# Kernel optimization log

Hardware: AMD Instinct MI355X
Metric: run time of the kernel (lower is better)

The kernel has to match this reference:

```python
import jax, jax.numpy as jnp
import numpy as np
import math

C = 1.0
IN_FEATURES = 512
SCALE = 1.0 / math.sqrt(IN_FEATURES)  # 1/sqrt(input_size) * lr_mul, lr_mul=1
LR_MUL = 1.0
GAIN = math.sqrt(2.0)
EPS = 1e-5       # clamp epsilon used by hyptorch-style pmath
PROJ_EPS = 1e-3  # boundary epsilon for project()


def _norm(x):
    return jnp.linalg.norm(x, axis=-1, keepdims=True)


def _artanh(x):
    return jnp.arctanh(jnp.clip(x, -1.0 + EPS, 1.0 - EPS))


def _project(x, c):
    sqrt_c = c ** 0.5
    norm = jnp.maximum(_norm(x), EPS)
    maxnorm = (1.0 - PROJ_EPS) / sqrt_c
    return jnp.where(norm > maxnorm, x / norm * maxnorm, x)


def _expmap0(u, c):
    sqrt_c = c ** 0.5
    u_norm = jnp.maximum(_norm(u), EPS)
    return jnp.tanh(sqrt_c * u_norm) * u / (sqrt_c * u_norm)


def _mobius_add(x, y, c):
    x2 = jnp.sum(x * x, axis=-1, keepdims=True)
    y2 = jnp.sum(y * y, axis=-1, keepdims=True)
    xy = jnp.sum(x * y, axis=-1, keepdims=True)
    num = (1.0 + 2.0 * c * xy + c * y2) * x + (1.0 - c * x2) * y
    denom = 1.0 + 2.0 * c * xy + c * c * x2 * y2
    return num / (denom + EPS)


def _mobius_matvec(m, x, c):
    # m: [out, in], x: [N, in]
    sqrt_c = c ** 0.5
    x_norm = jnp.maximum(_norm(x), EPS)
    mx = x @ m.T  # [N, out]
    mx_norm = jnp.maximum(_norm(mx), EPS)
    res = jnp.tanh(mx_norm / x_norm * _artanh(sqrt_c * x_norm)) * mx / (mx_norm * sqrt_c)
    zero_row = jnp.all(mx == 0, axis=-1, keepdims=True)
    return jnp.where(zero_row, jnp.zeros_like(res), res)


def _mobius_scalar_mult(x, r, c):
    sqrt_c = c ** 0.5
    x_norm = jnp.maximum(_norm(x), EPS)
    return jnp.tanh(r * _artanh(sqrt_c * x_norm)) * x / (x_norm * sqrt_c)


def setup_inputs() -> dict:
    key = jax.random.key(0)
    k1, k2, k3 = jax.random.split(key, 3)
    N, D_IN, D_OUT = 131072, 512, 512
    # scale x so points lie well inside the unit Poincare ball (norm ~ 0.45)
    x = jax.random.normal(k1, (N, D_IN), dtype=jnp.float32) * 0.02
    weight = jax.random.normal(k2, (D_OUT, D_IN), dtype=jnp.float32)
    bias = jax.random.normal(k3, (D_OUT,), dtype=jnp.float32) * 0.01
    return {"x": x, "weight": weight, "bias": bias}


def reference(x, weight, bias):
    c = C
    mv = _mobius_matvec(weight * SCALE, x, c)
    b = _expmap0(bias * LR_MUL, c)
    out = _project(_mobius_add(mv, b[None, :], c), c)
    out = jax.nn.leaky_relu(out, 0.2)
    out = _mobius_scalar_mult(out, GAIN, c)
    return out
```

## Files before the change

### kernel.cpp

```cpp
#include <hip/hip_runtime.h>
#include <math.h>

#define EPSV 1e-5f
#define SCALE_W 0.0441941738241592f
#define GAIN_R 1.4142135623730951f

typedef __attribute__((ext_vector_type(8))) short bf16x8;
typedef __attribute__((ext_vector_type(4))) float f32x4;

static __device__ __forceinline__ unsigned short f2bf(float f) {
  union { float f; unsigned int u; } v; v.f = f;
  unsigned int r = v.u + 0x7FFFu + ((v.u >> 16) & 1u);
  return (unsigned short)(r >> 16);
}

#define LBAR() do {                                          \
  asm volatile("s_waitcnt lgkmcnt(0)" ::: "memory");         \
  __builtin_amdgcn_sched_barrier(0);                         \
  __builtin_amdgcn_s_barrier();                              \
  __builtin_amdgcn_sched_barrier(0);                         \
  asm volatile("" ::: "memory");                             \
} while (0)

__global__ void bias_expmap_k(const float* __restrict__ bias, float* __restrict__ bexp,
                              float* __restrict__ y2out) {
  __shared__ float part[8];
  int t = threadIdx.x;
  float bv = bias[t];
  float s = bv * bv;
  s += __shfl_xor(s, 1);  s += __shfl_xor(s, 2);  s += __shfl_xor(s, 4);
  s += __shfl_xor(s, 8);  s += __shfl_xor(s, 16); s += __shfl_xor(s, 32);
  if ((t & 63) == 0) part[t >> 6] = s;
  __syncthreads();
  float tot = 0.f;
#pragma unroll
  for (int i = 0; i < 8; ++i) tot += part[i];
  float un = fmaxf(sqrtf(tot), EPSV);
  float th = tanhf(un);
  bexp[t] = th * bv / un;
  if (t == 0) *y2out = th * th;
}

__global__ void pack_weight_k(const float* __restrict__ w, unsigned short* __restrict__ wsB) {
  int e = blockIdx.x * 256 + threadIdx.x;
  int o = e >> 9;
  int k = e & 511;
  int ks = k >> 5, kk = k & 31;
  int lgr = kk >> 3, j = kk & 7;
  int colhi = o >> 4, l15 = o & 15;
  int dst = ((ks * 32 + colhi) * 64 + lgr * 16 + l15) * 8 + j;
  wsB[dst] = f2bf(w[e] * SCALE_W);
}

#define RB 80
#define KSROW 2560
#define BUFSZ 20480
#define SC_OFF 40960
#define SMEMSZ 43392

__global__ __launch_bounds__(512, 4)
void hyp_main_k(const float* __restrict__ x, const unsigned short* __restrict__ wsB,
                const float* __restrict__ bexp, const float* __restrict__ y2p,
                float* __restrict__ out, int tilesPerBlk) {
  extern __shared__ char smem[];
  const int tid  = threadIdx.x;
  const int lane = tid & 63;
  const int wave = tid >> 6;
  const int l15  = lane & 15;
  const int lgr  = lane >> 4;
  const int srow = tid >> 4;
  const int scol = tid & 15;

  float* xn2 = (float*)(smem + SC_OFF);
  float* pS2 = (float*)(smem + SC_OFF + 128);
  float* pSB = (float*)(smem + SC_OFF + 1152);
  float* g12 = (float*)(smem + SC_OFF + 2176);

  f32x4 bv4[4];
#pragma unroll
  for (int nf = 0; nf < 4; ++nf) bv4[nf] = *(const f32x4*)(bexp + wave * 64 + nf * 16 + lgr * 4);

  f32x4 acc[2][4];
#pragma unroll
  for (int mf = 0; mf < 2; ++mf)
#pragma unroll
    for (int nf = 0; nf < 4; ++nf) acc[mf][nf] = f32x4{0.f, 0.f, 0.f, 0.f};

  const char* ard0 = smem + l15 * RB + lgr * 16;
  const char* brd  = (const char*)wsB + ((wave * 4) * 64 + lane) * 16;
  char* awr0 = smem + srow * RB + (scol & 7) * 8;

  const long base = (long)blockIdx.x * tilesPerBlk;
  const int nss = 2 * tilesPerBlk;
  float xss = 0.f;
  f32x4 st[4];

  {
    const float* p = x + (size_t)(base * 32 + srow) * 512 + scol * 4;
#pragma unroll
    for (int i = 0; i < 4; ++i) st[i] = *(const f32x4*)(p + i * 64);
#pragma unroll
    for (int i = 0; i < 4; ++i) {
      f32x4 v = st[i];
      xss += v[0] * v[0] + v[1] * v[1] + v[2] * v[2] + v[3] * v[3];
      uint2 pk;
      pk.x = (unsigned int)f2bf(v[0]) | ((unsigned int)f2bf(v[1]) << 16);
      pk.y = (unsigned int)f2bf(v[2]) | ((unsigned int)f2bf(v[3]) << 16);
      *(uint2*)(awr0 + (2 * i + (scol >> 3)) * KSROW) = pk;
    }
  }
  LBAR();

  for (int s = 0; s < nss; ++s) {
    const int h = s & 1;
    const long tile = base + (s >> 1);
    const char* bufC = smem + (s & 1) * BUFSZ;

    if (s + 1 < nss) {
      const float* p = x + (size_t)((base + ((s + 1) >> 1)) * 32 + srow) * 512 +
                       ((s + 1) & 1) * 256 + scol * 4;
#pragma unroll
      for (int i = 0; i < 4; ++i) st[i] = *(const f32x4*)(p + i * 64);
    }

#pragma unroll
    for (int ks = 0; ks < 8; ++ks) {
      bf16x8 xf[2], wf[4];
#pragma unroll
      for (int mf = 0; mf < 2; ++mf)
        xf[mf] = *(const bf16x8*)(bufC + ks * KSROW + mf * (16 * RB) + (size_t)(ard0 - smem));
#pragma unroll
      for (int nf = 0; nf < 4; ++nf)
        wf[nf] = *(const bf16x8*)(brd + (size_t)(h * 8 + ks) * 32768 + nf * 1024);
#pragma unroll
      for (int mf = 0; mf < 2; ++mf)
#pragma unroll
        for (int nf = 0; nf < 4; ++nf)
          acc[mf][nf] = __builtin_amdgcn_mfma_f32_16x16x32_bf16(wf[nf], xf[mf], acc[mf][nf], 0, 0, 0);
    }

    if (h == 1) {
      float xs = xss;
      xs += __shfl_xor(xs, 1); xs += __shfl_xor(xs, 2);
      xs += __shfl_xor(xs, 4); xs += __shfl_xor(xs, 8);
      if (scol == 0) xn2[srow] = xs;
      xss = 0.f;

      float s2[2] = {0.f, 0.f}, sb[2] = {0.f, 0.f};
#pragma unroll
      for (int mf = 0; mf < 2; ++mf)
#pragma unroll
        for (int nf = 0; nf < 4; ++nf)
#pragma unroll
          for (int j = 0; j < 4; ++j) {
            float v = acc[mf][nf][j];
            s2[mf] += v * v;
            sb[mf] += v * bv4[nf][j];
          }
#pragma unroll
      for (int mf = 0; mf < 2; ++mf) {
        s2[mf] += __shfl_xor(s2[mf], 16); s2[mf] += __shfl_xor(s2[mf], 32);
        sb[mf] += __shfl_xor(sb[mf], 16); sb[mf] += __shfl_xor(sb[mf], 32);
      }
      if (lane < 16) {
#pragma unroll
        for (int mf = 0; mf < 2; ++mf) {
          pS2[(mf * 16 + l15) * 8 + wave] = s2[mf];
          pSB[(mf * 16 + l15) * 8 + wave] = sb[mf];
        }
      }
      LBAR();

      if (tid < 32) {
        int r = tid;
        float S2 = 0.f, SB = 0.f;
#pragma unroll
        for (int i = 0; i < 8; ++i) { S2 += pS2[r * 8 + i]; SB += pSB[r * 8 + i]; }
        float y2 = *y2p;
        float xn  = fmaxf(sqrtf(xn2[r]), EPSV);
        float mxn = fmaxf(sqrtf(S2), EPSV);
        float f = tanhf((mxn / xn) * atanhf(fminf(xn, 1.f - EPSV))) / mxn;
        float xy = f * SB;
        float x2 = f * f * S2;
        float den = 1.f + 2.f * xy + x2 * y2 + EPSV;
        float g1 = (1.f + 2.f * xy + y2) * f / den;
        float g2 = (1.f - x2) / den;
        float n1sq = g1 * g1 * S2 + 2.f * g1 * g2 * SB + g2 * g2 * y2;
        float n1 = fmaxf(sqrtf(fmaxf(n1sq, 0.f)), EPSV);
        if (n1 > 0.999f) { float sc = 0.999f / n1; g1 *= sc; g2 *= sc; }
        g12[r * 2] = g1; g12[r * 2 + 1] = g2;
      }
      LBAR();

      float n2p[2] = {0.f, 0.f};
#pragma unroll
      for (int mf = 0; mf < 2; ++mf) {
        float g1 = g12[(mf * 16 + l15) * 2], g2 = g12[(mf * 16 + l15) * 2 + 1];
#pragma unroll
        for (int nf = 0; nf < 4; ++nf)
#pragma unroll
          for (int j = 0; j < 4; ++j) {
            float v = g1 * acc[mf][nf][j] + g2 * bv4[nf][j];
            v = v > 0.f ? v : 0.2f * v;
            acc[mf][nf][j] = v;
            n2p[mf] += v * v;
          }
      }
#pragma unroll
      for (int mf = 0; mf < 2; ++mf) {
        n2p[mf] += __shfl_xor(n2p[mf], 16); n2p[mf] += __shfl_xor(n2p[mf], 32);
      }
      if (lane < 16) {
#pragma unroll
        for (int mf = 0; mf < 2; ++mf) pS2[(mf * 16 + l15) * 8 + wave] = n2p[mf];
      }
      LBAR();

      if (tid < 32) {
        int r = tid;
        float sn = 0.f;
#pragma unroll
        for (int i = 0; i < 8; ++i) sn += pS2[r * 8 + i];
        float n2 = fmaxf(sqrtf(sn), EPSV);
        xn2[r] = tanhf(GAIN_R * atanhf(fminf(n2, 1.f - EPSV))) / n2;
      }
      LBAR();

#pragma unroll
      for (int mf = 0; mf < 2; ++mf) {
        float tm = xn2[mf * 16 + l15];
#pragma unroll
        for (int nf = 0; nf < 4; ++nf) {
          f32x4 o = acc[mf][nf];
          o[0] *= tm; o[1] *= tm; o[2] *= tm; o[3] *= tm;
          *(f32x4*)(out + (size_t)(tile * 32 + mf * 16 + l15) * 512 +
                    wave * 64 + nf * 16 + lgr * 4) = o;
          acc[mf][nf] = f32x4{0.f, 0.f, 0.f, 0.f};
        }
      }
    }

    if (s + 1 < nss) {
      char* awr = smem + ((s + 1) & 1) * BUFSZ + (size_t)(awr0 - smem);
#pragma unroll
      for (int i = 0; i < 4; ++i) {
        f32x4 v = st[i];
        xss += v[0] * v[0] + v[1] * v[1] + v[2] * v[2] + v[3] * v[3];
        uint2 pk;
        pk.x = (unsigned int)f2bf(v[0]) | ((unsigned int)f2bf(v[1]) << 16);
        pk.y = (unsigned int)f2bf(v[2]) | ((unsigned int)f2bf(v[3]) << 16);
        *(uint2*)(awr + (2 * i + (scol >> 3)) * KSROW) = pk;
      }
    }
    LBAR();
  }
}

extern "C" void kernel_launch(void* const* d_in, const int* in_sizes, int n_in,
                              void* d_out, int out_size, void* d_ws, size_t ws_size,
                              hipStream_t stream) {
  const float* x    = (const float*)d_in[0];
  const float* w    = (const float*)d_in[1];
  const float* bias = (const float*)d_in[2];
  float* out = (float*)d_out;

  unsigned short* wsB = (unsigned short*)d_ws;
  float* bexp = (float*)((char*)d_ws + 524288);
  float* y2p  = (float*)((char*)d_ws + 524288 + 2048);

  bias_expmap_k<<<dim3(1), dim3(512), 0, stream>>>(bias, bexp, y2p);
  pack_weight_k<<<dim3(1024), dim3(256), 0, stream>>>(w, wsB);

  const int nrows  = in_sizes[0] / 512;
  const int ntiles = nrows / 32;
  const int nblk   = 1024;
  const int tpb    = ntiles / nblk;
  hyp_main_k<<<dim3(nblk), dim3(512), SMEMSZ, stream>>>(x, wsB, bexp, y2p, out, tpb);
}
```

Before: 180.9 us.

## Enlarge per-wave MFMA tile to 64 rows x 128 cols with 4-wave blocks

Restructures the main kernel so each block handles 64-row tiles using 4 waves of 256 threads. Each wave now computes a 64x128 output slab with a 4x8 accumulator grid, up from 32x64. The K dimension is split into four 128-wide stages instead of two. The goal is more reuse of each loaded weight fragment from global/L2 and of each x fragment from LDS per MFMA, cutting load traffic per flop. The cost is much higher register pressure (128 accumulator floats plus 8 staging vectors), fewer waves per CU, and half as many blocks for latency hiding.

```diff
diff --git a/kernel.cpp b/kernel.cpp
--- a/kernel.cpp
+++ b/kernel.cpp
@@ -53,12 +53,12 @@
 }
 
 #define RB 80
-#define KSROW 2560
+#define KSROW 5120
 #define BUFSZ 20480
 #define SC_OFF 40960
-#define SMEMSZ 43392
-
-__global__ __launch_bounds__(512, 4)
+#define SMEMSZ 43776
+
+__global__ __launch_bounds__(256, 2)
 void hyp_main_k(const float* __restrict__ x, const unsigned short* __restrict__ wsB,
                 const float* __restrict__ bexp, const float* __restrict__ y2p,
                 float* __restrict__ out, int tilesPerBlk) {
@@ -68,114 +68,115 @@
   const int wave = tid >> 6;
   const int l15  = lane & 15;
   const int lgr  = lane >> 4;
-  const int srow = tid >> 4;
-  const int scol = tid & 15;
+  const int srow = tid >> 2;
+  const int sq   = tid & 3;
 
   float* xn2 = (float*)(smem + SC_OFF);
-  float* pS2 = (float*)(smem + SC_OFF + 128);
-  float* pSB = (float*)(smem + SC_OFF + 1152);
-  float* g12 = (float*)(smem + SC_OFF + 2176);
-
-  f32x4 bv4[4];
-#pragma unroll
-  for (int nf = 0; nf < 4; ++nf) bv4[nf] = *(const f32x4*)(bexp + wave * 64 + nf * 16 + lgr * 4);
-
-  f32x4 acc[2][4];
-#pragma unroll
-  for (int mf = 0; mf < 2; ++mf)
-#pragma unroll
-    for (int nf = 0; nf < 4; ++nf) acc[mf][nf] = f32x4{0.f, 0.f, 0.f, 0.f};
+  float* pS2 = (float*)(smem + SC_OFF + 256);
+  float* pSB = (float*)(smem + SC_OFF + 1280);
+  float* g12 = (float*)(smem + SC_OFF + 2304);
 
   const char* ard0 = smem + l15 * RB + lgr * 16;
-  const char* brd  = (const char*)wsB + ((wave * 4) * 64 + lane) * 16;
-  char* awr0 = smem + srow * RB + (scol & 7) * 8;
+  const char* brd  = (const char*)wsB + ((size_t)(wave * 8) * 64 + lane) * 16;
+  char* awr0 = smem + sq * KSROW + srow * RB;
+
+  f32x4 acc[4][8];
+#pragma unroll
+  for (int mf = 0; mf < 4; ++mf)
+#pragma unroll
+    for (int nf = 0; nf < 8; ++nf) acc[mf][nf] = f32x4{0.f, 0.f, 0.f, 0.f};
 
   const long base = (long)blockIdx.x * tilesPerBlk;
-  const int nss = 2 * tilesPerBlk;
+  const int nss = 4 * tilesPerBlk;
   float xss = 0.f;
-  f32x4 st[4];
+  f32x4 st[8];
 
   {
-    const float* p = x + (size_t)(base * 32 + srow) * 512 + scol * 4;
-#pragma unroll
-    for (int i = 0; i < 4; ++i) st[i] = *(const f32x4*)(p + i * 64);
-#pragma unroll
-    for (int i = 0; i < 4; ++i) {
+    const float* p = x + (size_t)(base * 64 + srow) * 512 + sq * 32;
+#pragma unroll
+    for (int i = 0; i < 8; ++i) st[i] = *(const f32x4*)(p + i * 4);
+#pragma unroll
+    for (int i = 0; i < 8; ++i) {
       f32x4 v = st[i];
       xss += v[0] * v[0] + v[1] * v[1] + v[2] * v[2] + v[3] * v[3];
       uint2 pk;
       pk.x = (unsigned int)f2bf(v[0]) | ((unsigned int)f2bf(v[1]) << 16);
       pk.y = (unsigned int)f2bf(v[2]) | ((unsigned int)f2bf(v[3]) << 16);
-      *(uint2*)(awr0 + (2 * i + (scol >> 3)) * KSROW) = pk;
+      *(uint2*)(awr0 + i * 8) = pk;
     }
   }
   LBAR();
 
   for (int s = 0; s < nss; ++s) {
-    const int h = s & 1;
-    const long tile = base + (s >> 1);
-    const char* bufC = smem + (s & 1) * BUFSZ;
+    const int q = s & 3;
+    const int buf = s & 1;
 
     if (s + 1 < nss) {
-      const float* p = x + (size_t)((base + ((s + 1) >> 1)) * 32 + srow) * 512 +
-                       ((s + 1) & 1) * 256 + scol * 4;
-#pragma unroll
-      for (int i = 0; i < 4; ++i) st[i] = *(const f32x4*)(p + i * 64);
-    }
-
-#pragma unroll
-    for (int ks = 0; ks < 8; ++ks) {
-      bf16x8 xf[2], wf[4];
-#pragma unroll
-      for (int mf = 0; mf < 2; ++mf)
-        xf[mf] = *(const bf16x8*)(bufC + ks * KSROW + mf * (16 * RB) + (size_t)(ard0 - smem));
-#pragma unroll
-      for (int nf = 0; nf < 4; ++nf)
-        wf[nf] = *(const bf16x8*)(brd + (size_t)(h * 8 + ks) * 32768 + nf * 1024);
-#pragma unroll
-      for (int mf = 0; mf < 2; ++mf)
-#pragma unroll
-        for (int nf = 0; nf < 4; ++nf)
+      const int sp = s + 1;
+      const float* p = x + (size_t)((base + (sp >> 2)) * 64 + srow) * 512 + (sp & 3) * 128 + sq * 32;
+#pragma unroll
+      for (int i = 0; i < 8; ++i) st[i] = *(const f32x4*)(p + i * 4);
+    }
+
+#pragma unroll
+    for (int ksl = 0; ksl < 4; ++ksl) {
+      const int gks = q * 4 + ksl;
+      bf16x8 xf[4], wf[8];
+#pragma unroll
+      for (int mf = 0; mf < 4; ++mf)
+        xf[mf] = *(const bf16x8*)(ard0 + buf * BUFSZ + ksl * KSROW + mf * 1280);
+#pragma unroll
+      for (int nf = 0; nf < 8; ++nf)
+        wf[nf] = *(const bf16x8*)(brd + (size_t)gks * 32768 + nf * 1024);
+#pragma unroll
+      for (int mf = 0; mf < 4; ++mf)
+#pragma unroll
+        for (int nf = 0; nf < 8; ++nf)
           acc[mf][nf] = __builtin_amdgcn_mfma_f32_16x16x32_bf16(wf[nf], xf[mf], acc[mf][nf], 0, 0, 0);
     }
 
-    if (h == 1) {
+    if (q == 3) {
+      const long tile = base + (s >> 2);
+
       float xs = xss;
       xs += __shfl_xor(xs, 1); xs += __shfl_xor(xs, 2);
-      xs += __shfl_xor(xs, 4); xs += __shfl_xor(xs, 8);
-      if (scol == 0) xn2[srow] = xs;
+      if (sq == 0) xn2[srow] = xs;
       xss = 0.f;
 
-      float s2[2] = {0.f, 0.f}, sb[2] = {0.f, 0.f};
-#pragma unroll
-      for (int mf = 0; mf < 2; ++mf)
-#pragma unroll
-        for (int nf = 0; nf < 4; ++nf)
+      f32x4 bvv[8];
+#pragma unroll
+      for (int nf = 0; nf < 8; ++nf)
+        bvv[nf] = *(const f32x4*)(bexp + wave * 128 + nf * 16 + lgr * 4);
+
+      float s2[4], sb[4];
+#pragma unroll
+      for (int mf = 0; mf < 4; ++mf) {
+        s2[mf] = 0.f; sb[mf] = 0.f;
+#pragma unroll
+        for (int nf = 0; nf < 8; ++nf)
 #pragma unroll
           for (int j = 0; j < 4; ++j) {
             float v = acc[mf][nf][j];
             s2[mf] += v * v;
-            sb[mf] += v * bv4[nf][j];
+            sb[mf] += v * bvv[nf][j];
           }
-#pragma unroll
-      for (int mf = 0; mf < 2; ++mf) {
         s2[mf] += __shfl_xor(s2[mf], 16); s2[mf] += __shfl_xor(s2[mf], 32);
         sb[mf] += __shfl_xor(sb[mf], 16); sb[mf] += __shfl_xor(sb[mf], 32);
       }
       if (lane < 16) {
 #pragma unroll
-        for (int mf = 0; mf < 2; ++mf) {
-          pS2[(mf * 16 + l15) * 8 + wave] = s2[mf];
-          pSB[(mf * 16 + l15) * 8 + wave] = sb[mf];
+        for (int mf = 0; mf < 4; ++mf) {
+          pS2[(mf * 16 + l15) * 4 + wave] = s2[mf];
+          pSB[(mf * 16 + l15) * 4 + wave] = sb[mf];
         }
       }
       LBAR();
 
-      if (tid < 32) {
+      if (tid < 64) {
         int r = tid;
         float S2 = 0.f, SB = 0.f;
 #pragma unroll
-        for (int i = 0; i < 8; ++i) { S2 += pS2[r * 8 + i]; SB += pSB[r * 8 + i]; }
+        for (int i = 0; i < 4; ++i) { S2 += pS2[r * 4 + i]; SB += pSB[r * 4 + i]; }
         float y2 = *y2p;
         float xn  = fmaxf(sqrtf(xn2[r]), EPSV);
         float mxn = fmaxf(sqrtf(S2), EPSV);
@@ -192,64 +193,62 @@
       }
       LBAR();
 
-      float n2p[2] = {0.f, 0.f};
-#pragma unroll
-      for (int mf = 0; mf < 2; ++mf) {
+      float n2p[4];
+#pragma unroll
+      for (int mf = 0; mf < 4; ++mf) {
         float g1 = g12[(mf * 16 + l15) * 2], g2 = g12[(mf * 16 + l15) * 2 + 1];
-#pragma unroll
-        for (int nf = 0; nf < 4; ++nf)
+        n2p[mf] = 0.f;
+#pragma unroll
+        for (int nf = 0; nf < 8; ++nf)
 #pragma unroll
           for (int j = 0; j < 4; ++j) {
-            float v = g1 * acc[mf][nf][j] + g2 * bv4[nf][j];
+            float v = g1 * acc[mf][nf][j] + g2 * bvv[nf][j];
             v = v > 0.f ? v : 0.2f * v;
             acc[mf][nf][j] = v;
             n2p[mf] += v * v;
           }
-      }
-#pragma unroll
-      for (int mf = 0; mf < 2; ++mf) {
         n2p[mf] += __shfl_xor(n2p[mf], 16); n2p[mf] += __shfl_xor(n2p[mf], 32);
       }
       if (lane < 16) {
 #pragma unroll
-        for (int mf = 0; mf < 2; ++mf) pS2[(mf * 16 + l15) * 8 + wave] = n2p[mf];
-      }
-      LBAR();
-
-      if (tid < 32) {
+        for (int mf = 0; mf < 4; ++mf) pS2[(mf * 16 + l15) * 4 + wave] = n2p[mf];
+      }
+      LBAR();
+
+      if (tid < 64) {
         int r = tid;
         float sn = 0.f;
 #pragma unroll
-        for (int i = 0; i < 8; ++i) sn += pS2[r * 8 + i];
+        for (int i = 0; i < 4; ++i) sn += pS2[r * 4 + i];
         float n2 = fmaxf(sqrtf(sn), EPSV);
         xn2[r] = tanhf(GAIN_R * atanhf(fminf(n2, 1.f - EPSV))) / n2;
       }
       LBAR();
 
 #pragma unroll
-      for (int mf = 0; mf < 2; ++mf) {
+      for (int mf = 0; mf < 4; ++mf) {
         float tm = xn2[mf * 16 + l15];
 #pragma unroll
-        for (int nf = 0; nf < 4; ++nf) {
+        for (int nf = 0; nf < 8; ++nf) {
           f32x4 o = acc[mf][nf];
           o[0] *= tm; o[1] *= tm; o[2] *= tm; o[3] *= tm;
-          *(f32x4*)(out + (size_t)(tile * 32 + mf * 16 + l15) * 512 +
-                    wave * 64 + nf * 16 + lgr * 4) = o;
+          *(f32x4*)(out + (size_t)(tile * 64 + mf * 16 + l15) * 512 +
+                    wave * 128 + nf * 16 + lgr * 4) = o;
           acc[mf][nf] = f32x4{0.f, 0.f, 0.f, 0.f};
         }
       }
     }
 
     if (s + 1 < nss) {
-      char* awr = smem + ((s + 1) & 1) * BUFSZ + (size_t)(awr0 - smem);
-#pragma unroll
-      for (int i = 0; i < 4; ++i) {
+      char* awr = awr0 + ((s + 1) & 1) * BUFSZ;
+#pragma unroll
+      for (int i = 0; i < 8; ++i) {
         f32x4 v = st[i];
         xss += v[0] * v[0] + v[1] * v[1] + v[2] * v[2] + v[3] * v[3];
         uint2 pk;
         pk.x = (unsigned int)f2bf(v[0]) | ((unsigned int)f2bf(v[1]) << 16);
         pk.y = (unsigned int)f2bf(v[2]) | ((unsigned int)f2bf(v[3]) << 16);
-        *(uint2*)(awr + (2 * i + (scol >> 3)) * KSROW) = pk;
+        *(uint2*)(awr + i * 8) = pk;
       }
     }
     LBAR();
@@ -272,8 +271,8 @@
   pack_weight_k<<<dim3(1024), dim3(256), 0, stream>>>(w, wsB);
 
   const int nrows  = in_sizes[0] / 512;
-  const int ntiles = nrows / 32;
-  const int nblk   = 1024;
+  const int ntiles = nrows / 64;
+  const int nblk   = 512;
   const int tpb    = ntiles / nblk;
-  hyp_main_k<<<dim3(nblk), dim3(512), SMEMSZ, stream>>>(x, wsB, bexp, y2p, out, tpb);
-}
+  hyp_main_k<<<dim3(nblk), dim3(256), SMEMSZ, stream>>>(x, wsB, bexp, y2p, out, tpb);
+}
```

Measured after the change: 177.7 us. Within noise of the previous version (-1.8%).

## Double-buffer MFMA operand loads and stagger K-chunk order per block

Applied to the files above, without the earlier changes.

Operand fragments for the next K-step (weights from global memory, x from LDS) are now prefetched into a second register set while the current step's MFMAs run, with a sched_barrier separating the loads from the math. Each block also rotates its starting K-chunk by blockIdx and swaps which half of the input row it processes first, so concurrent blocks hit different weight addresses and different halves of x. The aim is to hide load latency and spread weight-read contention across memory channels, at the cost of more registers under the 512x4 launch bound. The memory clobber in the LDS barrier macro is also removed, which relaxes compiler ordering around LDS accesses.

```diff
diff --git a/kernel.cpp b/kernel.cpp
--- a/kernel.cpp
+++ b/kernel.cpp
@@ -19,7 +19,6 @@
   __builtin_amdgcn_sched_barrier(0);                         \
   __builtin_amdgcn_s_barrier();                              \
   __builtin_amdgcn_sched_barrier(0);                         \
-  asm volatile("" ::: "memory");                             \
 } while (0)
 
 __global__ void bias_expmap_k(const float* __restrict__ bias, float* __restrict__ bexp,
@@ -70,6 +69,8 @@
   const int lgr  = lane >> 4;
   const int srow = tid >> 4;
   const int scol = tid & 15;
+  const int rot   = blockIdx.x & 7;
+  const int hswap = (blockIdx.x >> 3) & 1;
 
   float* xn2 = (float*)(smem + SC_OFF);
   float* pS2 = (float*)(smem + SC_OFF + 128);
@@ -96,7 +97,7 @@
   f32x4 st[4];
 
   {
-    const float* p = x + (size_t)(base * 32 + srow) * 512 + scol * 4;
+    const float* p = x + (size_t)(base * 32 + srow) * 512 + hswap * 256 + scol * 4;
 #pragma unroll
     for (int i = 0; i < 4; ++i) st[i] = *(const f32x4*)(p + i * 64);
 #pragma unroll
@@ -113,30 +114,50 @@
 
   for (int s = 0; s < nss; ++s) {
     const int h = s & 1;
+    const int hcur = h ^ hswap;
     const long tile = base + (s >> 1);
     const char* bufC = smem + (s & 1) * BUFSZ;
+    const size_t hbase = (size_t)hcur * 8 * 32768;
+
+    bf16x8 wfb[2][4], xfb[2][2];
+    {
+      const int g0 = rot;
+#pragma unroll
+      for (int r = 0; r < 4; ++r)
+        wfb[0][r] = *(const bf16x8*)(brd + hbase + (size_t)g0 * 32768 + r * 1024);
+    }
 
     if (s + 1 < nss) {
-      const float* p = x + (size_t)((base + ((s + 1) >> 1)) * 32 + srow) * 512 +
-                       ((s + 1) & 1) * 256 + scol * 4;
+      const int sp = s + 1;
+      const float* p = x + (size_t)((base + (sp >> 1)) * 32 + srow) * 512 +
+                       (((sp & 1) ^ hswap)) * 256 + scol * 4;
 #pragma unroll
       for (int i = 0; i < 4; ++i) st[i] = *(const f32x4*)(p + i * 64);
     }
 
 #pragma unroll
+    for (int i = 0; i < 2; ++i)
+      xfb[0][i] = *(const bf16x8*)(bufC + rot * KSROW + i * 1280 + (size_t)(ard0 - smem));
+
+#pragma unroll
     for (int ks = 0; ks < 8; ++ks) {
-      bf16x8 xf[2], wf[4];
+      const int cb = ks & 1, nb = cb ^ 1;
+      if (ks < 7) {
+        const int gn = (ks + 1 + rot) & 7;
+#pragma unroll
+        for (int r = 0; r < 4; ++r)
+          wfb[nb][r] = *(const bf16x8*)(brd + hbase + (size_t)gn * 32768 + r * 1024);
+#pragma unroll
+        for (int i = 0; i < 2; ++i)
+          xfb[nb][i] = *(const bf16x8*)(bufC + gn * KSROW + i * 1280 + (size_t)(ard0 - smem));
+      }
+      __builtin_amdgcn_sched_barrier(0);
 #pragma unroll
       for (int mf = 0; mf < 2; ++mf)
-        xf[mf] = *(const bf16x8*)(bufC + ks * KSROW + mf * (16 * RB) + (size_t)(ard0 - smem));
-#pragma unroll
-      for (int nf = 0; nf < 4; ++nf)
-        wf[nf] = *(const bf16x8*)(brd + (size_t)(h * 8 + ks) * 32768 + nf * 1024);
-#pragma unroll
-      for (int mf = 0; mf < 2; ++mf)
 #pragma unroll
         for (int nf = 0; nf < 4; ++nf)
-          acc[mf][nf] = __builtin_amdgcn_mfma_f32_16x16x32_bf16(wf[nf], xf[mf], acc[mf][nf], 0, 0, 0);
+          acc[mf][nf] = __builtin_amdgcn_mfma_f32_16x16x32_bf16(wfb[cb][nf], xfb[cb][mf],
+                                                                acc[mf][nf], 0, 0, 0);
     }
 
     if (h == 1) {
@@ -241,7 +262,7 @@
     }
 
     if (s + 1 < nss) {
-      char* awr = smem + ((s + 1) & 1) * BUFSZ + (size_t)(awr0 - smem);
+      char* awr = awr0 + ((s + 1) & 1) * BUFSZ;
 #pragma unroll
       for (int i = 0; i < 4; ++i) {
         f32x4 v = st[i];
```

Result: slower. 214.5 us (+18.6%).
